# Kernel optimization log

Hardware: AMD Instinct MI355X
Metric: run time of the kernel (lower is better)

## Reference

```python
import jax, jax.numpy as jnp
import numpy as np

QUERY_DIM = 512
CAAN_DIM = 512
HID = 30

def setup_inputs() -> dict:
    key = jax.random.key(0)
    ks = jax.random.split(key, 9)
    def lin(kk, out_d, in_d):
        lim = 1.0 / np.sqrt(in_d)
        return jax.random.uniform(kk, (out_d, in_d), jnp.float32, -lim, lim)
    R = jax.random.normal(ks[0], (8, 2048, QUERY_DIM), jnp.float32)
    return {
        "R": R,
        "Wq": lin(ks[1], CAAN_DIM, QUERY_DIM), "bq": jnp.zeros((CAAN_DIM,), jnp.float32),
        "Wk": lin(ks[2], CAAN_DIM, QUERY_DIM), "bk": jnp.zeros((CAAN_DIM,), jnp.float32),
        "Wv": lin(ks[3], CAAN_DIM, QUERY_DIM), "bv": jnp.zeros((CAAN_DIM,), jnp.float32),
        "W1": lin(ks[4], HID, CAAN_DIM), "b1": jax.random.uniform(ks[5], (HID,), jnp.float32, -1/np.sqrt(CAAN_DIM), 1/np.sqrt(CAAN_DIM)),
        "W2": lin(ks[6], 1, HID), "b2": jax.random.uniform(ks[7], (1,), jnp.float32, -1/np.sqrt(HID), 1/np.sqrt(HID)),
    }

def reference(R, Wq, bq, Wk, bk, Wv, bv, W1, b1, W2, b2):
    # Projections: [b, n, d]
    Q = jnp.einsum('bnq,dq->bnd', R, Wq) + bq
    K = jnp.einsum('bnq,dq->bnd', R, Wk) + bk
    V = jnp.einsum('bnq,dq->bnd', R, Wv) + bv
    dk = K.shape[-1]
    # Full score matrix, naive exp-normalize (no max subtraction) as in original
    gamma = jnp.einsum('bnd,bmd->bnm', Q, K) / jnp.sqrt(jnp.float32(dk))
    e = jnp.exp(gamma)
    saat = e / jnp.sum(e, axis=2, keepdims=True)  # [b, n, n]
    a = jnp.einsum('bnm,bmd->bnd', saat, V)       # [b, n, d]
    # fc head: CAAN_dim -> 30 -> 1, squeeze last dim
    h = jnp.einsum('bnd,hd->bnh', a, W1) + b1
    winner_score = (jnp.einsum('bnh,oh->bno', h, W2) + b2)[..., 0]
    return winner_score
```

## Files before the change

### kernel.cpp

```cpp
#include <hip/hip_runtime.h>
#include <math.h>

#define BATCH 8
#define SEQ 2048
#define DIM 512
#define MTOT (BATCH*SEQ)
#define HID 30

typedef short bf16x8 __attribute__((ext_vector_type(8)));
typedef float f32x4 __attribute__((ext_vector_type(4)));

__device__ __forceinline__ unsigned short f2bf(float f) {
  unsigned int u = __float_as_uint(f);
  unsigned int r = (u + 0x7FFFu + ((u >> 16) & 1u)) >> 16;
  return (unsigned short)r;
}
__device__ __forceinline__ float bf2f(unsigned short u) {
  return __uint_as_float((unsigned int)u << 16);
}

__device__ __forceinline__ void gload_lds16(const void* g, void* l) {
  __builtin_amdgcn_global_load_lds((const __attribute__((address_space(1))) void*)g,
                                   (__attribute__((address_space(3))) void*)l, 16, 0, 0);
}

__device__ __forceinline__ void gemm256_core(const unsigned short* __restrict__ gA,
                                             const unsigned short* __restrict__ gB,
                                             char* smem, f32x4 (&acc)[8][4]) {
  const int t = threadIdx.x;
  const int lane = t & 63;
  const int w = t >> 6;
  const int wr = w >> 2, wc = w & 3;
  const int lr = lane & 15, kc = lane >> 4;
  const int ss = (t & 7) ^ ((t >> 3) & 7);
  const unsigned short* gsrc = (ss < 4 ? gA : gB) + (size_t)(t >> 3) * DIM + (ss & 3) * 8;
  const uint32_t dbase = (uint32_t)(t & 448) * 16;

  auto stage = [&](int slot, int kt) {
#pragma unroll
    for (int q = 0; q < 4; ++q)
      gload_lds16(gsrc + (size_t)(q * 64) * DIM + kt * 32,
                  smem + slot * 32768 + q * 8192 + dbase);
  };

  stage(0, 0); stage(1, 1);
  asm volatile("s_waitcnt vmcnt(4)" ::: "memory");
  __builtin_amdgcn_s_barrier();
  asm volatile("" ::: "memory");

#pragma unroll
  for (int kt = 0; kt < 16; ++kt) {
    const char* Ab = smem + (kt % 3) * 32768;
    const int fslot = (kt + 2) % 3;
    const int src = (kt + 2 < 16) ? (kt + 2) : 15;
    bf16x8 bfr[4], af[4], af2[4];
#pragma unroll
    for (int j = 0; j < 4; ++j) {
      int r = wc * 64 + j * 16 + lr;
      bfr[j] = *(const bf16x8*)(Ab + r * 128 + (((4 + kc) ^ (r & 7)) << 4));
    }
#pragma unroll
    for (int i = 0; i < 4; ++i) {
      int r = wr * 128 + i * 16 + lr;
      af[i] = *(const bf16x8*)(Ab + r * 128 + ((kc ^ (r & 7)) << 4));
    }
    __builtin_amdgcn_sched_barrier(0);
#pragma unroll
    for (int i = 0; i < 4; ++i) {
      int r = wr * 128 + (i + 4) * 16 + lr;
      af2[i] = *(const bf16x8*)(Ab + r * 128 + ((kc ^ (r & 7)) << 4));
    }
    __builtin_amdgcn_sched_barrier(0);
    stage(fslot, src);
    __builtin_amdgcn_sched_barrier(0);
    __builtin_amdgcn_s_setprio(1);
#pragma unroll
    for (int i = 0; i < 4; ++i)
#pragma unroll
      for (int j = 0; j < 4; ++j)
        acc[i][j] = __builtin_amdgcn_mfma_f32_16x16x32_bf16(af[i], bfr[j], acc[i][j], 0, 0, 0);
    __builtin_amdgcn_s_setprio(0);
    __builtin_amdgcn_sched_barrier(0);
    __builtin_amdgcn_s_setprio(1);
#pragma unroll
    for (int i = 0; i < 4; ++i)
#pragma unroll
      for (int j = 0; j < 4; ++j)
        acc[i + 4][j] = __builtin_amdgcn_mfma_f32_16x16x32_bf16(af2[i], bfr[j], acc[i + 4][j], 0, 0, 0);
    __builtin_amdgcn_s_setprio(0);
    __builtin_amdgcn_sched_barrier(0);
    asm volatile("s_waitcnt vmcnt(4)" ::: "memory");
    __builtin_amdgcn_s_barrier();
    asm volatile("" ::: "memory");
  }
}

__global__ __launch_bounds__(256) void k_prep(
    const float* __restrict__ R, const float* __restrict__ Wq, const float* __restrict__ Wk,
    const float* __restrict__ Wv, const float* __restrict__ bq, const float* __restrict__ bv,
    const float* __restrict__ W1, const float* __restrict__ b1,
    const float* __restrict__ W2, const float* __restrict__ b2,
    unsigned short* __restrict__ Gt, unsigned short* __restrict__ Rb16,
    float* __restrict__ u, float* __restrict__ wv2, float* __restrict__ consts) {
  __shared__ __align__(16) float As[16][34];
  __shared__ __align__(16) float Bs[16][34];
  __shared__ float vecs[512];
  __shared__ float red2[16][17];
  const int bid = blockIdx.x;
  const int t = threadIdx.x;

  if (bid >= 321) {
    size_t base = ((size_t)(bid - 321) * 256 + t) * 8;
    float4 r0 = *(const float4*)&R[base];
    float4 r1 = *(const float4*)&R[base + 4];
    ushort4 lo, hi;
    lo.x = f2bf(r0.x); lo.y = f2bf(r0.y); lo.z = f2bf(r0.z); lo.w = f2bf(r0.w);
    hi.x = f2bf(r1.x); hi.y = f2bf(r1.y); hi.z = f2bf(r1.z); hi.w = f2bf(r1.w);
    *(ushort4*)&Rb16[base] = lo;
    *(ushort4*)&Rb16[base + 4] = hi;
    return;
  }
  if (bid < 256) {
    int tm = t & 15, tn = t >> 4;
    int q1b = (bid & 15) * 32, q2b = (bid >> 4) * 32;
    int lk = t >> 4, lc = (t & 15) * 2;
    float acc[2][2] = {};
    float2 ra = *(const float2*)&Wq[(size_t)lk * DIM + q1b + lc];
    float2 rb = *(const float2*)&Wk[(size_t)lk * DIM + q2b + lc];
    for (int kb = 0; kb < DIM; kb += 16) {
      *(float2*)&As[lk][lc] = ra;
      *(float2*)&Bs[lk][lc] = rb;
      __syncthreads();
      if (kb + 16 < DIM) {
        ra = *(const float2*)&Wq[(size_t)(kb + 16 + lk) * DIM + q1b + lc];
        rb = *(const float2*)&Wk[(size_t)(kb + 16 + lk) * DIM + q2b + lc];
      }
#pragma unroll
      for (int k = 0; k < 16; ++k) {
        float a0 = As[k][tm * 2], a1 = As[k][tm * 2 + 1];
        float b0 = Bs[k][tn * 2], b1v = Bs[k][tn * 2 + 1];
        acc[0][0] = fmaf(a0, b0, acc[0][0]); acc[0][1] = fmaf(a0, b1v, acc[0][1]);
        acc[1][0] = fmaf(a1, b0, acc[1][0]); acc[1][1] = fmaf(a1, b1v, acc[1][1]);
      }
      __syncthreads();
    }
#pragma unroll
    for (int i = 0; i < 2; ++i)
#pragma unroll
      for (int j = 0; j < 2; ++j)
        Gt[(size_t)(q2b + tn * 2 + j) * DIM + (q1b + tm * 2 + i)] = f2bf(acc[i][j]);
    return;
  }
  if (bid < 320) {
    bool isU = bid < 288;
    int qb = (bid - (isU ? 256 : 288)) * 16;
    if (isU) {
      vecs[t] = bq[t];
      vecs[t + 256] = bq[t + 256];
    } else {
      for (int d = t; d < DIM; d += 256) {
        float s = 0.f;
        for (int j = 0; j < HID; ++j) s = fmaf(W2[j], W1[(size_t)j * DIM + d], s);
        vecs[d] = s;
      }
    }
    __syncthreads();
    const float* M = isU ? Wk : Wv;
    int ql = t & 15, ds = t >> 4;
    float s = 0.f;
#pragma unroll 8
    for (int i = 0; i < 32; ++i) {
      int d = ds * 32 + i;
      s = fmaf(vecs[d], M[(size_t)d * DIM + qb + ql], s);
    }
    red2[ds][ql] = s;
    __syncthreads();
    if (t < 16) {
      float r = 0.f;
#pragma unroll
      for (int k = 0; k < 16; ++k) r += red2[k][t];
      (isU ? u : wv2)[qb + t] = r;
    }
    return;
  }
  {
    for (int d = t; d < DIM; d += 256) {
      float s = 0.f;
      for (int j = 0; j < HID; ++j) s = fmaf(W2[j], W1[(size_t)j * DIM + d], s);
      vecs[d] = s;
    }
    __syncthreads();
    float* red = (float*)red2;
    red[t] = bv[t] * vecs[t] + bv[t + 256] * vecs[t + 256];
    __syncthreads();
    for (int o = 128; o > 0; o >>= 1) {
      if (t < o) red[t] += red[t + o];
      __syncthreads();
    }
    if (t == 0) {
      consts[0] = red[0];
      float s = b2[0];
      for (int j = 0; j < HID; ++j) s = fmaf(W2[j], b1[j], s);
      consts[1] = s;
    }
  }
}

__global__ __launch_bounds__(512, 2) void k_projT(const unsigned short* __restrict__ Rb16,
                                                  const unsigned short* __restrict__ Gt,
                                                  const float* __restrict__ u,
                                                  const float* __restrict__ wv2,
                                                  unsigned short* __restrict__ Tb16,
                                                  float* __restrict__ vw) {
  __shared__ __align__(16) char smem[98304];
  __shared__ float u_lds[256];
  int t = threadIdx.x;
  size_t rowb = (size_t)blockIdx.x * 256;
  int colb = blockIdx.y * 256;
  if (t < 256) u_lds[t] = u[colb + t];
  f32x4 acc[8][4] = {};
  gemm256_core(Rb16 + rowb * DIM, Gt + (size_t)colb * DIM, smem, acc);
  int lane = t & 63, w = t >> 6, wr = w >> 2, wc = w & 3;
  int lr = lane & 15, kq = lane >> 4;
#pragma unroll
  for (int i = 0; i < 8; ++i)
#pragma unroll
    for (int j = 0; j < 4; ++j)
#pragma unroll
      for (int r = 0; r < 4; ++r) {
        int row = wr * 128 + i * 16 + kq * 4 + r;
        int col = wc * 64 + j * 16 + lr;
        Tb16[(rowb + row) * DIM + colb + col] = f2bf(acc[i][j][r] + u_lds[col]);
      }
  if (blockIdx.y == 0) {
    asm volatile("s_waitcnt vmcnt(0)" ::: "memory");
    __syncthreads();
    float* wv2s = (float*)smem;
    wv2s[t] = wv2[t];
    __syncthreads();
    int row = (int)rowb + (t >> 1);
    const unsigned short* rp = Rb16 + (size_t)row * DIM + (t & 1) * 256;
    const float* wp = wv2s + (t & 1) * 256;
    float s = 0.f;
#pragma unroll 8
    for (int i = 0; i < 32; ++i) {
      bf16x8 v = *(const bf16x8*)(rp + i * 8);
#pragma unroll
      for (int e = 0; e < 8; ++e) s = fmaf(bf2f((unsigned short)v[e]), wp[i * 8 + e], s);
    }
    s += __shfl_xor(s, 1);
    if ((t & 1) == 0) vw[row] = s;
  }
}

__global__ __launch_bounds__(512, 2) void k_qk(const unsigned short* __restrict__ Tb16,
                                               const unsigned short* __restrict__ Rb16,
                                               const float* __restrict__ vw,
                                               float* __restrict__ part_s1,
                                               float* __restrict__ part_den) {
  __shared__ __align__(16) char smem[98304];
  __shared__ float vw_lds[256];
  __shared__ float red_s1[4][256], red_den[4][256];
  int t = threadIdx.x;
  int orig = blockIdx.x;
  int wgid = (orig & 7) * 64 + (orig >> 3);
  int b = wgid >> 6;
  int nb = ((wgid >> 3) & 7) * 256;
  int mb = (wgid & 7) * 256;
  if (t < 256) vw_lds[t] = vw[b * SEQ + mb + t];
  f32x4 acc[8][4] = {};
  gemm256_core(Tb16 + ((size_t)b * SEQ + nb) * DIM,
               Rb16 + ((size_t)b * SEQ + mb) * DIM, smem, acc);
  int lane = t & 63, w = t >> 6, wr = w >> 2, wc = w & 3;
  int lr = lane & 15, kq = lane >> 4;
  const float rs = 0.044194173824159216f;
  float vwl[4];
#pragma unroll
  for (int j = 0; j < 4; ++j) vwl[j] = vw_lds[wc * 64 + j * 16 + lr];
#pragma unroll
  for (int i = 0; i < 8; ++i) {
#pragma unroll
    for (int r = 0; r < 4; ++r) {
      float sa = 0.f, sd = 0.f;
#pragma unroll
      for (int j = 0; j < 4; ++j) {
        float e = __expf(acc[i][j][r] * rs);
        sa = fmaf(e, vwl[j], sa);
        sd += e;
      }
#pragma unroll
      for (int m = 1; m < 16; m <<= 1) { sa += __shfl_xor(sa, m); sd += __shfl_xor(sd, m); }
      if (lr == 0) {
        int rl = wr * 128 + i * 16 + kq * 4 + r;
        red_s1[wc][rl] = sa;
        red_den[wc][rl] = sd;
      }
    }
  }
  __syncthreads();
  if (t < 256) {
    size_t o = ((size_t)b * 8 + (mb >> 8)) * SEQ + nb + t;
    part_s1[o] = red_s1[0][t] + red_s1[1][t] + red_s1[2][t] + red_s1[3][t];
    part_den[o] = red_den[0][t] + red_den[1][t] + red_den[2][t] + red_den[3][t];
  }
}

__global__ void k_final(const float* __restrict__ part_s1, const float* __restrict__ part_den,
                        const float* __restrict__ consts, float* __restrict__ out) {
  int n = blockIdx.x * 256 + threadIdx.x;
  int b = n >> 11, nn = n & 2047;
  float s1 = 0.f, dn = 0.f;
#pragma unroll
  for (int i = 0; i < 8; ++i) {
    size_t o = ((size_t)b * 8 + i) * SEQ + nn;
    s1 += part_s1[o];
    dn += part_den[o];
  }
  out[n] = s1 / dn + consts[0] + consts[1];
}

extern "C" void kernel_launch(void* const* d_in, const int* in_sizes, int n_in,
                              void* d_out, int out_size, void* d_ws, size_t ws_size,
                              hipStream_t stream) {
  const float* R  = (const float*)d_in[0];
  const float* Wq = (const float*)d_in[1];
  const float* bq = (const float*)d_in[2];
  const float* Wk = (const float*)d_in[3];
  const float* bk = (const float*)d_in[4];
  const float* Wv = (const float*)d_in[5];
  const float* bv = (const float*)d_in[6];
  const float* W1 = (const float*)d_in[7];
  const float* b1 = (const float*)d_in[8];
  const float* W2 = (const float*)d_in[9];
  const float* b2 = (const float*)d_in[10];
  (void)bk;
  float* out = (float*)d_out;

  char* p = (char*)d_ws;
  unsigned short* Rb16 = (unsigned short*)p; p += (size_t)MTOT * DIM * 2;
  unsigned short* Tb16 = (unsigned short*)p; p += (size_t)MTOT * DIM * 2;
  unsigned short* Gt   = (unsigned short*)p; p += (size_t)DIM * DIM * 2;
  float* part_s1  = (float*)p; p += (size_t)BATCH * 8 * SEQ * 4;
  float* part_den = (float*)p; p += (size_t)BATCH * 8 * SEQ * 4;
  float* u      = (float*)p; p += DIM * 4;
  float* wv2    = (float*)p; p += DIM * 4;
  float* vw     = (float*)p; p += MTOT * 4;
  float* consts = (float*)p; p += 16;

  hipLaunchKernelGGL(k_prep, dim3(321 + MTOT * DIM / (256 * 8)), dim3(256), 0, stream,
                     R, Wq, Wk, Wv, bq, bv, W1, b1, W2, b2, Gt, Rb16, u, wv2, consts);
  hipLaunchKernelGGL(k_projT, dim3(MTOT / 256, DIM / 256), dim3(512), 0, stream,
                     Rb16, Gt, u, wv2, Tb16, vw);
  hipLaunchKernelGGL(k_qk, dim3(512), dim3(512), 0, stream, Tb16, Rb16, vw, part_s1, part_den);
  hipLaunchKernelGGL(k_final, dim3(MTOT / 256), dim3(256), 0, stream,
                     part_s1, part_den, consts, out);
}
```

Before: 93.07 us.

## Replace QK GEMM core with eight-phase double-buffered pipelined schedule

Adds a new bf16 MFMA GEMM core for the score kernel. It uses 64-wide K tiles, double-buffered A and B tiles in 128KB of LDS, and staggers the global-to-LDS loads across eight phases per iteration. The phases are separated by explicit waitcnt and barrier points, with raised priority around the MFMA bursts. The goal is to hide load latency behind matrix math and cut stalls. In exchange it uses more LDS and fragile hand-tuned wait counts, which could limit occupancy or add barrier overhead.

```diff
diff --git a/kernel.cpp b/kernel.cpp
--- a/kernel.cpp
+++ b/kernel.cpp
@@ -22,6 +22,91 @@
 __device__ __forceinline__ void gload_lds16(const void* g, void* l) {
   __builtin_amdgcn_global_load_lds((const __attribute__((address_space(1))) void*)g,
                                    (__attribute__((address_space(3))) void*)l, 16, 0, 0);
+}
+
+__device__ __forceinline__ void gemm256_8ph(const unsigned short* __restrict__ gA,
+                                            const unsigned short* __restrict__ gB,
+                                            char* smem, f32x4 (&acc)[8][4]) {
+  const int t = threadIdx.x;
+  const int lane = t & 63;
+  const int w = t >> 6;
+  const int wr = w >> 2, wc = w & 3;
+  const int lr = lane & 15, kc = lane >> 4;
+  const int ss = (t & 7) ^ ((t >> 3) & 7);
+  const size_t srcoff = (size_t)(t >> 3) * DIM + ss * 8;
+  const uint32_t dst = (uint32_t)t * 16;
+
+  auto stageH = [&](int d, int M, int kt, int h) {
+    const unsigned short* g = (M ? gB : gA) + srcoff + ((size_t)h * 128) * DIM + kt * 64;
+    char* dest = smem + d * 65536 + M * 32768 + h * 16384 + dst;
+    gload_lds16(g, dest);
+    gload_lds16(g + (size_t)64 * DIM, dest + 8192);
+  };
+
+  stageH(0, 0, 0, 0); stageH(0, 0, 0, 1);
+  stageH(0, 1, 0, 0); stageH(0, 1, 0, 1);
+  stageH(1, 1, 1, 0); stageH(1, 1, 1, 1);
+  asm volatile("s_waitcnt vmcnt(4)" ::: "memory");
+  __builtin_amdgcn_s_barrier();
+  asm volatile("" ::: "memory");
+
+  bf16x8 bfr[2][4];
+#pragma unroll
+  for (int it = 0; it < 4; ++it) {
+#pragma unroll
+    for (int ph = 0; ph < 8; ++ph) {
+      const int d = ph >> 2;
+      const int q = ph & 3;
+      const char* Ab = smem + d * 65536;
+      const char* Bb = Ab + 32768;
+      bf16x8 af[2][2];
+      if (q == 0) {
+#pragma unroll
+        for (int s = 0; s < 2; ++s)
+#pragma unroll
+          for (int j = 0; j < 4; ++j) {
+            int r = wc * 64 + j * 16 + lr;
+            bfr[s][j] = *(const bf16x8*)(Bb + r * 128 + (((s * 4 + kc) ^ (r & 7)) << 4));
+          }
+      }
+#pragma unroll
+      for (int i2 = 0; i2 < 2; ++i2)
+#pragma unroll
+        for (int s = 0; s < 2; ++s) {
+          int r = wr * 128 + (2 * q + i2) * 16 + lr;
+          af[i2][s] = *(const bf16x8*)(Ab + r * 128 + (((s * 4 + kc) ^ (r & 7)) << 4));
+        }
+      __builtin_amdgcn_sched_barrier(0);
+      if (ph == 0) { stageH(1, 0, 2 * it + 1, 0); stageH(1, 0, 2 * it + 1, 1); }
+      if (it < 3) {
+        if (ph == 2) stageH(0, 1, 2 * it + 2, 0);
+        if (ph == 3) stageH(0, 1, 2 * it + 2, 1);
+        if (ph == 4) { stageH(0, 0, 2 * it + 2, 0); stageH(0, 0, 2 * it + 2, 1); }
+        if (ph == 6) stageH(1, 1, 2 * it + 3, 0);
+        if (ph == 7) stageH(1, 1, 2 * it + 3, 1);
+      }
+      __builtin_amdgcn_sched_barrier(0);
+      if (q == 0) asm volatile("s_waitcnt lgkmcnt(8)" ::: "memory");
+      __builtin_amdgcn_s_barrier();
+      asm volatile("s_waitcnt lgkmcnt(0)" ::: "memory");
+      __builtin_amdgcn_sched_barrier(0);
+      __builtin_amdgcn_s_setprio(1);
+#pragma unroll
+      for (int i2 = 0; i2 < 2; ++i2)
+#pragma unroll
+        for (int s = 0; s < 2; ++s)
+#pragma unroll
+          for (int j = 0; j < 4; ++j)
+            acc[2 * q + i2][j] = __builtin_amdgcn_mfma_f32_16x16x32_bf16(
+                af[i2][s], bfr[s][j], acc[2 * q + i2][j], 0, 0, 0);
+      __builtin_amdgcn_s_setprio(0);
+      __builtin_amdgcn_sched_barrier(0);
+      if (ph == 3 || ph == 7)
+        asm volatile("s_waitcnt vmcnt(4)" ::: "memory");
+      __builtin_amdgcn_s_barrier();
+      asm volatile("" ::: "memory");
+    }
+  }
 }
 
 __device__ __forceinline__ void gemm256_core(const unsigned short* __restrict__ gA,
@@ -258,7 +343,7 @@
                                                const float* __restrict__ vw,
                                                float* __restrict__ part_s1,
                                                float* __restrict__ part_den) {
-  __shared__ __align__(16) char smem[98304];
+  __shared__ __align__(16) char smem[131072];
   __shared__ float vw_lds[256];
   __shared__ float red_s1[4][256], red_den[4][256];
   int t = threadIdx.x;
@@ -269,8 +354,8 @@
   int mb = (wgid & 7) * 256;
   if (t < 256) vw_lds[t] = vw[b * SEQ + mb + t];
   f32x4 acc[8][4] = {};
-  gemm256_core(Tb16 + ((size_t)b * SEQ + nb) * DIM,
-               Rb16 + ((size_t)b * SEQ + mb) * DIM, smem, acc);
+  gemm256_8ph(Tb16 + ((size_t)b * SEQ + nb) * DIM,
+              Rb16 + ((size_t)b * SEQ + mb) * DIM, smem, acc);
   int lane = t & 63, w = t >> 6, wr = w >> 2, wc = w & 3;
   int lr = lane & 15, kq = lane >> 4;
   const float rs = 0.044194173824159216f;
```

Result: no change. 91.92 us (-1.2%).
